# Optimization experiments

Hardware: AMD Instinct MI355X
Metric: run time of the kernel (lower is better)

Reference implementation:

```python
import jax, jax.numpy as jnp
import numpy as np

D = 1024          # embeddings_dims
HS = 128          # head_size = D // no_of_q_heads(=8)
NKV = 2           # hardcoded self.no_of_kv_heads = 2 (number of query Linear layers)


def apply_rope(x):
    # x: [..., T, d]; pairs of adjacent elements rotated (faithful to RotaryEmbeddings)
    d = x.shape[-1]
    T = x.shape[-2]
    positions = jnp.arange(0, d, 2, dtype=jnp.float32)           # step-2 positions (as in source)
    theta = 10000.0 ** (-2.0 * positions / d)                    # [d/2]
    angles = jnp.arange(T, dtype=jnp.float32)[:, None] * theta[None, :]  # [T, d/2]
    cos, sin = jnp.cos(angles), jnp.sin(angles)
    xr = x.reshape(x.shape[:-1] + (d // 2, 2))
    out = jnp.stack([xr[..., 0] * cos - xr[..., 1] * sin,
                     xr[..., 1] * cos + xr[..., 0] * sin], axis=-1)
    return out.reshape(x.shape)


def setup_inputs() -> dict:
    key = jax.random.key(0)
    k1, k2, k3, k4, k5 = jax.random.split(key, 5)
    B, T = 4, 2048
    x = jax.random.normal(k1, (B, T, D), dtype=jnp.float32)
    s = 1.0 / np.sqrt(D)
    Wq = jax.random.normal(k2, (NKV, HS, D), dtype=jnp.float32) * s  # 2 query Linear layers [out,in]
    Wk = jax.random.normal(k3, (HS, D), dtype=jnp.float32) * s
    Wv = jax.random.normal(k4, (HS, D), dtype=jnp.float32) * s
    Wo = jax.random.normal(k5, (D, NKV * HS), dtype=jnp.float32) * (1.0 / np.sqrt(NKV * HS))
    return {"x": x, "Wq": Wq, "Wk": Wk, "Wv": Wv, "Wo": Wo}


def reference(x, Wq, Wk, Wv, Wo):
    B, T, _ = x.shape
    k = apply_rope(x @ Wk.T)                              # [B,T,HS]
    v = x @ Wv.T                                          # [B,T,HS]
    q = jnp.einsum('btd,hkd->bhtk', x, Wq)                # [B,2,T,HS]
    q = apply_rope(q)
    scale = HS ** (-0.5)
    scores = jnp.einsum('bhtk,bsk->bhts', q, k) * scale   # [B,2,T,T]
    causal = jnp.tril(jnp.ones((T, T), dtype=bool))
    scores = jnp.where(causal, scores, -jnp.inf)
    w = jax.nn.softmax(scores, axis=-1)                   # dropout is identity at eval
    out = jnp.einsum('bhts,bsk->bhtk', w, v)              # [B,2,T,HS]
    out = out.transpose(0, 2, 1, 3).reshape(B, T, NKV * HS)  # concat heads on last dim
    return out @ Wo.T                                     # [B,T,D]
```

## Files before the change

### kernel.cpp

```cpp
#include <hip/hip_runtime.h>
#include <math.h>

#define DD 1024
#define HSZ 128
#define NB 4
#define TT 2048

typedef __attribute__((ext_vector_type(8))) short bf16x8;
typedef __attribute__((ext_vector_type(4))) float f32x4;

typedef __attribute__((address_space(3))) unsigned int lds_u32_t;
typedef __attribute__((address_space(1))) unsigned int glb_u32_t;

__device__ inline void gll16(const void* g, void* l) {
    __builtin_amdgcn_global_load_lds((const glb_u32_t*)g, (lds_u32_t*)l, 16, 0, 0);
}

__device__ inline unsigned short f2bf(float f){
    unsigned u = __builtin_bit_cast(unsigned, f);
    u += 0x7fff + ((u >> 16) & 1);
    return (unsigned short)(u >> 16);
}

__global__ __launch_bounds__(256) void prep_kernel(
    const float* __restrict__ Wq, const float* __restrict__ Wk,
    const float* __restrict__ Wv, const float* __restrict__ Wo,
    unsigned short* __restrict__ Wbp, unsigned short* __restrict__ Wop,
    float2* __restrict__ tab)
{
    int bid = blockIdx.x, tid = threadIdx.x;
    if (bid < 512) {
        int i = bid * 256 + tid;
        int t = i >> 6, j = i & 63;
        float theta = __powf(10000.f, -(float)j * (1.f / 32.f));
        float ang = (float)t * theta;
        tab[i] = make_float2(__cosf(ang), __sinf(ang));
        return;
    }
    const float* s;
    unsigned short* dst;
    if (bid < 768) {
        int gc = (bid - 512) * 256 + tid;
        int tileid = gc >> 10;
        int ct = tileid >> 4, kk = tileid & 15;
        int ch = gc & 1023;
        int ns = ch >> 7, kc = (ch >> 6) & 1, l6 = ch & 63;
        int wrow = ct * 128 + ns * 16 + (l6 & 15);
        int kcol = kk * 64 + kc * 32 + (l6 >> 4) * 8;
        s = (wrow < 256) ? Wq + (size_t)wrow * DD
          : (wrow < 384) ? Wk + (size_t)(wrow - 256) * DD
                         : Wv + (size_t)(wrow - 384) * DD;
        s += kcol;
        dst = Wbp + (size_t)gc * 8;
    } else {
        int gc = (bid - 768) * 256 + tid;
        int tileid = gc >> 10;
        int ct = tileid >> 2, kk = tileid & 3;
        int ch = gc & 1023;
        int ns = ch >> 7, kc = (ch >> 6) & 1, l6 = ch & 63;
        int orow = ct * 128 + ns * 16 + (l6 & 15);
        int kcol = kk * 64 + kc * 32 + (l6 >> 4) * 8;
        s = Wo + (size_t)orow * 256 + kcol;
        dst = Wop + (size_t)gc * 8;
    }
    float4 a = ((const float4*)s)[0];
    float4 c = ((const float4*)s)[1];
    unsigned short o[8] = {f2bf(a.x),f2bf(a.y),f2bf(a.z),f2bf(a.w),
                           f2bf(c.x),f2bf(c.y),f2bf(c.z),f2bf(c.w)};
    *(uint4*)dst = *(const uint4*)o;
}

__global__ __launch_bounds__(256) void qkv_gemm_kernel(
    const float* __restrict__ x,
    const unsigned short* __restrict__ Wbp,
    const float2* __restrict__ tab,
    unsigned short* __restrict__ qo,
    unsigned short* __restrict__ Kp,
    unsigned short* __restrict__ Vp)
{
    int bid = blockIdx.x;
    int rt = bid & 127, ct = bid >> 7;
    int row0 = rt * 64;
    int b = row0 >> 11, t0 = row0 & (TT - 1);
    int tid = threadIdx.x;
    int wave = tid >> 6, lane = tid & 63;
    int mrow = lane & 15, quad = lane >> 4;

    __shared__ unsigned short Bs[2][8192];

    f32x4 acc[8];
    #pragma unroll
    for (int ns = 0; ns < 8; ++ns)
        #pragma unroll
        for (int r = 0; r < 4; ++r) acc[ns][r] = 0.f;

    const float* xrow = x + (size_t)(row0 + wave * 16 + mrow) * DD;

    {
        const unsigned short* wt = Wbp + (size_t)(ct * 16) * 8192;
        #pragma unroll
        for (int u = 0; u < 4; ++u)
            gll16(wt + (size_t)(u * 256 + tid) * 8, &Bs[0][(u * 256 + (tid & 192)) * 8]);
    }

    for (int kk = 0; kk < 16; ++kk) {
        __syncthreads();
        if (kk < 15) {
            const unsigned short* wt = Wbp + (size_t)(ct * 16 + kk + 1) * 8192;
            #pragma unroll
            for (int u = 0; u < 4; ++u)
                gll16(wt + (size_t)(u * 256 + tid) * 8, &Bs[(kk + 1) & 1][(u * 256 + (tid & 192)) * 8]);
        }
        bf16x8 af[2];
        #pragma unroll
        for (int kc = 0; kc < 2; ++kc) {
            const float* s = xrow + kk * 64 + kc * 32 + quad * 8;
            float4 f0 = ((const float4*)s)[0];
            float4 f1 = ((const float4*)s)[1];
            bf16x8 pk;
            pk[0]=(short)f2bf(f0.x); pk[1]=(short)f2bf(f0.y); pk[2]=(short)f2bf(f0.z); pk[3]=(short)f2bf(f0.w);
            pk[4]=(short)f2bf(f1.x); pk[5]=(short)f2bf(f1.y); pk[6]=(short)f2bf(f1.z); pk[7]=(short)f2bf(f1.w);
            af[kc] = pk;
        }
        const unsigned short* Bcur = Bs[kk & 1];
        #pragma unroll
        for (int kc = 0; kc < 2; ++kc)
            #pragma unroll
            for (int ns = 0; ns < 8; ++ns) {
                bf16x8 bb = *(const bf16x8*)(Bcur + ((ns * 2 + kc) * 64 + lane) * 8);
                acc[ns] = __builtin_amdgcn_mfma_f32_16x16x32_bf16(af[kc], bb, acc[ns], 0, 0, 0);
            }
    }

    __syncthreads();

    if (ct < 2) {
        unsigned short* dst = qo + (size_t)(b * 2 + ct) * TT * HSZ;
        #pragma unroll
        for (int ns = 0; ns < 8; ++ns) {
            int colloc = ns * 16 + mrow;
            int pj = colloc >> 1;
            #pragma unroll
            for (int r = 0; r < 4; ++r) {
                int t = t0 + wave * 16 + quad * 4 + r;
                float v = acc[ns][r];
                float vp = __shfl_xor(v, 1, 64);
                float2 cs = tab[t * 64 + pj];
                float outv = ((mrow & 1) == 0) ? (v * cs.x - vp * cs.y)
                                               : (v * cs.x + vp * cs.y);
                dst[(size_t)t * HSZ + colloc] = f2bf(outv);
            }
        }
    } else if (ct == 2) {
        unsigned short* A_ = (unsigned short*)Bs;
        #pragma unroll
        for (int ns = 0; ns < 8; ++ns) {
            int colloc = ns * 16 + mrow;
            int pj = colloc >> 1;
            int chunk = (ns >> 1) * 4 + wave;
            int lph = (ns & 1) * 2 + (mrow >> 3);
            #pragma unroll
            for (int r = 0; r < 4; ++r) {
                int t = t0 + wave * 16 + quad * 4 + r;
                float v = acc[ns][r];
                float vp = __shfl_xor(v, 1, 64);
                float2 cs = tab[t * 64 + pj];
                float outv = ((mrow & 1) == 0) ? (v * cs.x - vp * cs.y)
                                               : (v * cs.x + vp * cs.y);
                A_[chunk * 512 + (lph * 16 + quad * 4 + r) * 8 + (mrow & 7)] = f2bf(outv);
            }
        }
        __syncthreads();
        unsigned short* kd = Kp + (size_t)(b * 32 + (t0 >> 6)) * 8192;
        #pragma unroll
        for (int u = 0; u < 4; ++u)
            *(uint4*)(kd + (u * 256 + tid) * 8) = *(const uint4*)(A_ + (u * 256 + tid) * 8);
    } else {
        unsigned short* A_ = (unsigned short*)Bs;
        #pragma unroll
        for (int ns = 0; ns < 8; ++ns) {
            int chunk = ns * 2 + (wave >> 1);
            int lanep = ((wave & 1) * 2 + (quad >> 1)) * 16 + mrow;
            #pragma unroll
            for (int r = 0; r < 4; ++r)
                A_[chunk * 512 + lanep * 8 + (quad & 1) * 4 + r] = f2bf(acc[ns][r]);
        }
        __syncthreads();
        unsigned short* vd = Vp + (size_t)(b * 32 + (t0 >> 6)) * 8192;
        #pragma unroll
        for (int u = 0; u < 4; ++u)
            *(uint4*)(vd + (u * 256 + tid) * 8) = *(const uint4*)(A_ + (u * 256 + tid) * 8);
    }
}

__global__ __launch_bounds__(256) void attn_mfma_kernel(
    const unsigned short* __restrict__ q,
    const unsigned short* __restrict__ Kp,
    const unsigned short* __restrict__ Vp,
    unsigned short* __restrict__ att)
{
    int bid = blockIdx.x;
    int rr = bid >> 3;
    int qt = (rr < 32) ? rr : 63 - (rr - 32);
    int bh = bid & 7;
    int b = bh >> 1, h = bh & 1;
    int q0 = qt * 32;
    int tid = threadIdx.x;
    int wave = tid >> 6, lane = tid & 63;
    int qsub = wave >> 1, par = wave & 1;
    int qw0 = q0 + qsub * 16;
    int mrow = lane & 15, quad = lane >> 4;

    __shared__ char raw[74240];
    unsigned short* Ks0 = (unsigned short*)raw;
    unsigned short* Vs0 = (unsigned short*)(raw + 32768);
    unsigned short* Psb = (unsigned short*)(raw + 65536);
    float* Ms_ = (float*)(raw + 73728);
    float* Ls_ = Ms_ + 32;
    float* Os  = (float*)raw;

    const unsigned short* qrow = q + (((size_t)(b * 2 + h)) * TT + qw0 + mrow) * HSZ + quad * 8;
    bf16x8 qf[4];
    #pragma unroll
    for (int c = 0; c < 4; ++c) qf[c] = *(const bf16x8*)(qrow + 32 * c);

    float mrun[4], lrun[4];
    f32x4 O[8];
    #pragma unroll
    for (int r = 0; r < 4; ++r) { mrun[r] = -1e30f; lrun[r] = 0.f; }
    #pragma unroll
    for (int g = 0; g < 8; ++g)
        #pragma unroll
        for (int r = 0; r < 4; ++r) O[g][r] = 0.f;

    const int NT = (qt + 2) >> 1;
    const float scl = 0.08838834764831845f;

    for (int jj = 0; jj < NT; jj += 2) {
        __syncthreads();
        for (int tp = 0; tp < 2; ++tp) {
            int j = jj + tp;
            if (j >= NT) break;
            const unsigned short* ks = Kp + (size_t)(b * 32 + j) * 8192;
            const unsigned short* vs = Vp + (size_t)(b * 32 + j) * 8192;
            #pragma unroll
            for (int u = 0; u < 4; ++u) {
                gll16(ks + (size_t)(u * 256 + tid) * 8, Ks0 + (tp * 8192) + (u * 256 + (tid & 192)) * 8);
                gll16(vs + (size_t)(u * 256 + tid) * 8, Vs0 + (tp * 8192) + (u * 256 + (tid & 192)) * 8);
            }
        }
        __syncthreads();

        int j = jj + par;
        int s0 = j * 64;
        if (j < NT && s0 <= qw0 + 15) {
            const unsigned short* Kt = Ks0 + par * 8192;
            const unsigned short* Vtt = Vs0 + par * 8192;

            f32x4 S[4];
            #pragma unroll
            for (int f = 0; f < 4; ++f)
                #pragma unroll
                for (int r = 0; r < 4; ++r) S[f][r] = 0.f;

            #pragma unroll
            for (int c = 0; c < 4; ++c)
                #pragma unroll
                for (int f = 0; f < 4; ++f) {
                    bf16x8 bk = *(const bf16x8*)(Kt + ((c * 4 + f) * 64 + lane) * 8);
                    S[f] = __builtin_amdgcn_mfma_f32_16x16x32_bf16(qf[c], bk, S[f], 0, 0, 0);
                }

            #pragma unroll
            for (int f = 0; f < 4; ++f) {
                int sg = s0 + 16 * f + mrow;
                #pragma unroll
                for (int r = 0; r < 4; ++r) {
                    int qg = qw0 + quad * 4 + r;
                    float val = S[f][r] * scl;
                    S[f][r] = (sg <= qg) ? val : -1e30f;
                }
            }

            float al[4];
            #pragma unroll
            for (int r = 0; r < 4; ++r) {
                float v = fmaxf(fmaxf(S[0][r], S[1][r]), fmaxf(S[2][r], S[3][r]));
                v = fmaxf(v, __shfl_xor(v, 1, 64));
                v = fmaxf(v, __shfl_xor(v, 2, 64));
                v = fmaxf(v, __shfl_xor(v, 4, 64));
                v = fmaxf(v, __shfl_xor(v, 8, 64));
                float mn = fmaxf(mrun[r], v);
                al[r] = __expf(mrun[r] - mn);
                mrun[r] = mn;
            }
            #pragma unroll
            for (int f = 0; f < 4; ++f)
                #pragma unroll
                for (int r = 0; r < 4; ++r)
                    S[f][r] = __expf(S[f][r] - mrun[r]);
            #pragma unroll
            for (int r = 0; r < 4; ++r) {
                float v = (S[0][r] + S[1][r]) + (S[2][r] + S[3][r]);
                v += __shfl_xor(v, 1, 64);
                v += __shfl_xor(v, 2, 64);
                v += __shfl_xor(v, 4, 64);
                v += __shfl_xor(v, 8, 64);
                lrun[r] = lrun[r] * al[r] + v;
            }
            #pragma unroll
            for (int g = 0; g < 8; ++g) {
                O[g][0] *= al[0]; O[g][1] *= al[1]; O[g][2] *= al[2]; O[g][3] *= al[3];
            }

            unsigned short* Pw = Psb + wave * 1024;
            #pragma unroll
            for (int f = 0; f < 4; ++f) {
                int p = f >> 1;
                int hi2 = (2 * f + (mrow >> 3)) & 3;
                int jlo = mrow & 7;
                #pragma unroll
                for (int r = 0; r < 4; ++r)
                    Pw[(p * 64 + hi2 * 16 + quad * 4 + r) * 8 + jlo] = f2bf(S[f][r]);
            }
            bf16x8 pa[2];
            pa[0] = *(const bf16x8*)(Pw + lane * 8);
            pa[1] = *(const bf16x8*)(Pw + (64 + lane) * 8);

            #pragma unroll
            for (int g = 0; g < 8; ++g)
                #pragma unroll
                for (int p = 0; p < 2; ++p) {
                    bf16x8 bv = *(const bf16x8*)(Vtt + ((g * 2 + p) * 64 + lane) * 8);
                    O[g] = __builtin_amdgcn_mfma_f32_16x16x32_bf16(pa[p], bv, O[g], 0, 0, 0);
                }
        }
    }

    __syncthreads();
    if (par == 1) {
        if (mrow == 0) {
            #pragma unroll
            for (int r = 0; r < 4; ++r) {
                Ms_[qsub * 16 + quad * 4 + r] = mrun[r];
                Ls_[qsub * 16 + quad * 4 + r] = lrun[r];
            }
        }
        float* Ow = Os + qsub * 2048;
        #pragma unroll
        for (int g = 0; g < 8; ++g)
            #pragma unroll
            for (int r = 0; r < 4; ++r)
                Ow[(quad * 4 + r) * 128 + g * 16 + mrow] = O[g][r];
    }
    __syncthreads();
    if (par == 0) {
        const float* Op = Os + qsub * 2048;
        float A0[4], A1[4], inv[4];
        #pragma unroll
        for (int r = 0; r < 4; ++r) {
            float m1 = Ms_[qsub * 16 + quad * 4 + r];
            float l1 = Ls_[qsub * 16 + quad * 4 + r];
            float m12 = fmaxf(mrun[r], m1);
            A0[r] = __expf(mrun[r] - m12);
            A1[r] = __expf(m1 - m12);
            inv[r] = 1.f / (lrun[r] * A0[r] + l1 * A1[r]);
        }
        unsigned short* ab = att + (((size_t)b * TT + qw0) * 2 + h) * 128;
        #pragma unroll
        for (int g = 0; g < 8; ++g)
            #pragma unroll
            for (int r = 0; r < 4; ++r) {
                int row = quad * 4 + r;
                float o = (O[g][r] * A0[r] + Op[row * 128 + g * 16 + mrow] * A1[r]) * inv[r];
                ab[(size_t)row * 256 + g * 16 + mrow] = f2bf(o);
            }
    }
}

__global__ __launch_bounds__(256) void outproj_gemm_kernel(
    const unsigned short* __restrict__ attb,
    const unsigned short* __restrict__ Wop,
    float* __restrict__ y)
{
    int bid = blockIdx.x;
    int rt = bid & 127, ct = bid >> 7;
    int row0 = rt * 64;
    int tid = threadIdx.x;
    int wave = tid >> 6, lane = tid & 63;
    int mrow = lane & 15, quad = lane >> 4;

    __shared__ unsigned short Bs[2][8192];

    f32x4 acc[8];
    #pragma unroll
    for (int ns = 0; ns < 8; ++ns)
        #pragma unroll
        for (int r = 0; r < 4; ++r) acc[ns][r] = 0.f;

    const unsigned short* arow = attb + (size_t)(row0 + wave * 16 + mrow) * 256;

    {
        const unsigned short* wt = Wop + (size_t)(ct * 4) * 8192;
        #pragma unroll
        for (int u = 0; u < 4; ++u)
            gll16(wt + (size_t)(u * 256 + tid) * 8, &Bs[0][(u * 256 + (tid & 192)) * 8]);
    }

    for (int kk = 0; kk < 4; ++kk) {
        __syncthreads();
        if (kk < 3) {
            const unsigned short* wt = Wop + (size_t)(ct * 4 + kk + 1) * 8192;
            #pragma unroll
            for (int u = 0; u < 4; ++u)
                gll16(wt + (size_t)(u * 256 + tid) * 8, &Bs[(kk + 1) & 1][(u * 256 + (tid & 192)) * 8]);
        }
        const unsigned short* Bcur = Bs[kk & 1];
        #pragma unroll
        for (int kc = 0; kc < 2; ++kc) {
            bf16x8 af = *(const bf16x8*)(arow + kk * 64 + kc * 32 + quad * 8);
            #pragma unroll
            for (int ns = 0; ns < 8; ++ns) {
                bf16x8 bb = *(const bf16x8*)(Bcur + ((ns * 2 + kc) * 64 + lane) * 8);
                acc[ns] = __builtin_amdgcn_mfma_f32_16x16x32_bf16(af, bb, acc[ns], 0, 0, 0);
            }
        }
    }

    #pragma unroll
    for (int ns = 0; ns < 8; ++ns)
        #pragma unroll
        for (int r = 0; r < 4; ++r) {
            int row = row0 + wave * 16 + quad * 4 + r;
            y[(size_t)row * DD + ct * 128 + ns * 16 + mrow] = acc[ns][r];
        }
}

extern "C" void kernel_launch(void* const* d_in, const int* in_sizes, int n_in,
                              void* d_out, int out_size, void* d_ws, size_t ws_size,
                              hipStream_t stream) {
    const float* x  = (const float*)d_in[0];
    const float* Wq = (const float*)d_in[1];
    const float* Wk = (const float*)d_in[2];
    const float* Wv = (const float*)d_in[3];
    const float* Wo = (const float*)d_in[4];
    float* y = (float*)d_out;

    char* ws = (char*)d_ws;
    unsigned short* at  = (unsigned short*)(ws);
    unsigned short* qo  = (unsigned short*)(ws + 4u  * 1024 * 1024);
    unsigned short* Kp  = (unsigned short*)(ws + 8u  * 1024 * 1024);
    unsigned short* Vp  = (unsigned short*)(ws + 10u * 1024 * 1024);
    unsigned short* Wbp = (unsigned short*)(ws + 12u * 1024 * 1024);
    unsigned short* Wop = (unsigned short*)(ws + 13u * 1024 * 1024);
    float2*         tb  = (float2*)        (ws + 13824u * 1024);

    prep_kernel<<<896, 256, 0, stream>>>(Wq, Wk, Wv, Wo, Wbp, Wop, tb);
    qkv_gemm_kernel<<<512, 256, 0, stream>>>(x, Wbp, tb, qo, Kp, Vp);
    attn_mfma_kernel<<<512, 256, 0, stream>>>(qo, Kp, Vp, at);
    outproj_gemm_kernel<<<1024, 256, 0, stream>>>(at, Wop, y);
}
```

Baseline: 169.6 us.

## Split attention KV tiles across four waves, each covering 32 query rows

The attention kernel now assigns key/value tiles round-robin to the four waves, and each wave handles all 32 query rows of the block. Each wave reads K and V tiles straight from global memory instead of staging them through LDS, which removes the per-iteration block-wide barriers. Partial softmax results from the four waves are merged through LDS at the end. The block order now runs from the longest query tile to the shortest, the causal mask is applied only on the last tile, and the launch bounds request two blocks per CU. The cost is more registers per wave, redundant global reads of K/V with no LDS reuse, and a four-way final merge.

```diff
diff --git a/kernel.cpp b/kernel.cpp
--- a/kernel.cpp
+++ b/kernel.cpp
@@ -193,127 +193,127 @@
     }
 }
 
-__global__ __launch_bounds__(256) void attn_mfma_kernel(
+__global__ __launch_bounds__(256, 2) void attn_mfma_kernel(
     const unsigned short* __restrict__ q,
     const unsigned short* __restrict__ Kp,
     const unsigned short* __restrict__ Vp,
     unsigned short* __restrict__ att)
 {
     int bid = blockIdx.x;
-    int rr = bid >> 3;
-    int qt = (rr < 32) ? rr : 63 - (rr - 32);
+    int qt = 63 - (bid >> 3);
     int bh = bid & 7;
     int b = bh >> 1, h = bh & 1;
     int q0 = qt * 32;
     int tid = threadIdx.x;
     int wave = tid >> 6, lane = tid & 63;
-    int qsub = wave >> 1, par = wave & 1;
-    int qw0 = q0 + qsub * 16;
     int mrow = lane & 15, quad = lane >> 4;
 
-    __shared__ char raw[74240];
-    unsigned short* Ks0 = (unsigned short*)raw;
-    unsigned short* Vs0 = (unsigned short*)(raw + 32768);
-    unsigned short* Psb = (unsigned short*)(raw + 65536);
-    float* Ms_ = (float*)(raw + 73728);
-    float* Ls_ = Ms_ + 32;
-    float* Os  = (float*)raw;
-
-    const unsigned short* qrow = q + (((size_t)(b * 2 + h)) * TT + qw0 + mrow) * HSZ + quad * 8;
-    bf16x8 qf[4];
+    __shared__ char raw[66304];
+    unsigned short* Psb = (unsigned short*)raw;
+    float* Os  = (float*)(raw + 16384);
+    float* Ms_ = (float*)(raw + 65536);
+    float* Ls_ = Ms_ + 96;
+
+    const unsigned short* qbase = q + (((size_t)(b * 2 + h)) * TT + q0 + mrow) * HSZ + quad * 8;
+    bf16x8 qf[2][4];
     #pragma unroll
-    for (int c = 0; c < 4; ++c) qf[c] = *(const bf16x8*)(qrow + 32 * c);
-
-    float mrun[4], lrun[4];
-    f32x4 O[8];
+    for (int u = 0; u < 2; ++u)
+        #pragma unroll
+        for (int c = 0; c < 4; ++c)
+            qf[u][c] = *(const bf16x8*)(qbase + u * 16 * HSZ + 32 * c);
+
+    float mrun[2][4], lrun[2][4];
+    f32x4 O[2][8];
     #pragma unroll
-    for (int r = 0; r < 4; ++r) { mrun[r] = -1e30f; lrun[r] = 0.f; }
-    #pragma unroll
-    for (int g = 0; g < 8; ++g)
-        #pragma unroll
-        for (int r = 0; r < 4; ++r) O[g][r] = 0.f;
-
-    const int NT = (qt + 2) >> 1;
+    for (int u = 0; u < 2; ++u) {
+        #pragma unroll
+        for (int r = 0; r < 4; ++r) { mrun[u][r] = -1e30f; lrun[u][r] = 0.f; }
+        #pragma unroll
+        for (int g = 0; g < 8; ++g)
+            #pragma unroll
+            for (int r = 0; r < 4; ++r) O[u][g][r] = 0.f;
+    }
+
+    const int NT = (qt >> 1) + 1;
     const float scl = 0.08838834764831845f;
-
-    for (int jj = 0; jj < NT; jj += 2) {
-        __syncthreads();
-        for (int tp = 0; tp < 2; ++tp) {
-            int j = jj + tp;
-            if (j >= NT) break;
-            const unsigned short* ks = Kp + (size_t)(b * 32 + j) * 8192;
-            const unsigned short* vs = Vp + (size_t)(b * 32 + j) * 8192;
-            #pragma unroll
-            for (int u = 0; u < 4; ++u) {
-                gll16(ks + (size_t)(u * 256 + tid) * 8, Ks0 + (tp * 8192) + (u * 256 + (tid & 192)) * 8);
-                gll16(vs + (size_t)(u * 256 + tid) * 8, Vs0 + (tp * 8192) + (u * 256 + (tid & 192)) * 8);
-            }
-        }
-        __syncthreads();
-
-        int j = jj + par;
+    unsigned short* Pw = Psb + wave * 2048;
+
+    for (int j = wave; j < NT; j += 4) {
+        const unsigned short* Kt = Kp + (size_t)(b * 32 + j) * 8192;
+        const unsigned short* Vt = Vp + (size_t)(b * 32 + j) * 8192;
         int s0 = j * 64;
-        if (j < NT && s0 <= qw0 + 15) {
-            const unsigned short* Kt = Ks0 + par * 8192;
-            const unsigned short* Vtt = Vs0 + par * 8192;
-
-            f32x4 S[4];
+
+        f32x4 S[2][4];
+        #pragma unroll
+        for (int u = 0; u < 2; ++u)
             #pragma unroll
             for (int f = 0; f < 4; ++f)
                 #pragma unroll
-                for (int r = 0; r < 4; ++r) S[f][r] = 0.f;
-
-            #pragma unroll
-            for (int c = 0; c < 4; ++c)
+                for (int r = 0; r < 4; ++r) S[u][f][r] = 0.f;
+
+        #pragma unroll
+        for (int c = 0; c < 4; ++c)
+            #pragma unroll
+            for (int f = 0; f < 4; ++f) {
+                bf16x8 bk = *(const bf16x8*)(Kt + ((c * 4 + f) * 64 + lane) * 8);
+                S[0][f] = __builtin_amdgcn_mfma_f32_16x16x32_bf16(qf[0][c], bk, S[0][f], 0, 0, 0);
+                S[1][f] = __builtin_amdgcn_mfma_f32_16x16x32_bf16(qf[1][c], bk, S[1][f], 0, 0, 0);
+            }
+
+        if (j == NT - 1) {
+            #pragma unroll
+            for (int u = 0; u < 2; ++u)
                 #pragma unroll
                 for (int f = 0; f < 4; ++f) {
-                    bf16x8 bk = *(const bf16x8*)(Kt + ((c * 4 + f) * 64 + lane) * 8);
-                    S[f] = __builtin_amdgcn_mfma_f32_16x16x32_bf16(qf[c], bk, S[f], 0, 0, 0);
+                    int sg = s0 + 16 * f + mrow;
+                    #pragma unroll
+                    for (int r = 0; r < 4; ++r) {
+                        int qg = q0 + u * 16 + quad * 4 + r;
+                        S[u][f][r] = (sg <= qg) ? S[u][f][r] * scl : -1e30f;
+                    }
                 }
-
-            #pragma unroll
-            for (int f = 0; f < 4; ++f) {
-                int sg = s0 + 16 * f + mrow;
-                #pragma unroll
-                for (int r = 0; r < 4; ++r) {
-                    int qg = qw0 + quad * 4 + r;
-                    float val = S[f][r] * scl;
-                    S[f][r] = (sg <= qg) ? val : -1e30f;
-                }
-            }
-
+        } else {
+            #pragma unroll
+            for (int u = 0; u < 2; ++u)
+                #pragma unroll
+                for (int f = 0; f < 4; ++f)
+                    #pragma unroll
+                    for (int r = 0; r < 4; ++r) S[u][f][r] *= scl;
+        }
+
+        #pragma unroll
+        for (int u = 0; u < 2; ++u) {
             float al[4];
             #pragma unroll
             for (int r = 0; r < 4; ++r) {
-                float v = fmaxf(fmaxf(S[0][r], S[1][r]), fmaxf(S[2][r], S[3][r]));
+                float v = fmaxf(fmaxf(S[u][0][r], S[u][1][r]), fmaxf(S[u][2][r], S[u][3][r]));
                 v = fmaxf(v, __shfl_xor(v, 1, 64));
                 v = fmaxf(v, __shfl_xor(v, 2, 64));
                 v = fmaxf(v, __shfl_xor(v, 4, 64));
                 v = fmaxf(v, __shfl_xor(v, 8, 64));
-                float mn = fmaxf(mrun[r], v);
-                al[r] = __expf(mrun[r] - mn);
-                mrun[r] = mn;
+                float mn = fmaxf(mrun[u][r], v);
+                al[r] = __expf(mrun[u][r] - mn);
+                mrun[u][r] = mn;
             }
             #pragma unroll
             for (int f = 0; f < 4; ++f)
                 #pragma unroll
                 for (int r = 0; r < 4; ++r)
-                    S[f][r] = __expf(S[f][r] - mrun[r]);
+                    S[u][f][r] = __expf(S[u][f][r] - mrun[u][r]);
             #pragma unroll
             for (int r = 0; r < 4; ++r) {
-                float v = (S[0][r] + S[1][r]) + (S[2][r] + S[3][r]);
+                float v = (S[u][0][r] + S[u][1][r]) + (S[u][2][r] + S[u][3][r]);
                 v += __shfl_xor(v, 1, 64);
                 v += __shfl_xor(v, 2, 64);
                 v += __shfl_xor(v, 4, 64);
                 v += __shfl_xor(v, 8, 64);
-                lrun[r] = lrun[r] * al[r] + v;
+                lrun[u][r] = lrun[u][r] * al[r] + v;
             }
             #pragma unroll
             for (int g = 0; g < 8; ++g) {
-                O[g][0] *= al[0]; O[g][1] *= al[1]; O[g][2] *= al[2]; O[g][3] *= al[3];
-            }
-
-            unsigned short* Pw = Psb + wave * 1024;
+                O[u][g][0] *= al[0]; O[u][g][1] *= al[1];
+                O[u][g][2] *= al[2]; O[u][g][3] *= al[3];
+            }
             #pragma unroll
             for (int f = 0; f < 4; ++f) {
                 int p = f >> 1;
@@ -321,60 +321,76 @@
                 int jlo = mrow & 7;
                 #pragma unroll
                 for (int r = 0; r < 4; ++r)
-                    Pw[(p * 64 + hi2 * 16 + quad * 4 + r) * 8 + jlo] = f2bf(S[f][r]);
-            }
-            bf16x8 pa[2];
-            pa[0] = *(const bf16x8*)(Pw + lane * 8);
-            pa[1] = *(const bf16x8*)(Pw + (64 + lane) * 8);
-
+                    Pw[u * 1024 + (p * 64 + hi2 * 16 + quad * 4 + r) * 8 + jlo] = f2bf(S[u][f][r]);
+            }
+        }
+
+        bf16x8 pa[2][2];
+        #pragma unroll
+        for (int u = 0; u < 2; ++u)
+            #pragma unroll
+            for (int p = 0; p < 2; ++p)
+                pa[u][p] = *(const bf16x8*)(Pw + u * 1024 + (p * 64 + lane) * 8);
+
+        #pragma unroll
+        for (int g = 0; g < 8; ++g)
+            #pragma unroll
+            for (int p = 0; p < 2; ++p) {
+                bf16x8 bv = *(const bf16x8*)(Vt + ((g * 2 + p) * 64 + lane) * 8);
+                O[0][g] = __builtin_amdgcn_mfma_f32_16x16x32_bf16(pa[0][p], bv, O[0][g], 0, 0, 0);
+                O[1][g] = __builtin_amdgcn_mfma_f32_16x16x32_bf16(pa[1][p], bv, O[1][g], 0, 0, 0);
+            }
+    }
+
+    if (wave) {
+        float* Ow = Os + (wave - 1) * 4096;
+        #pragma unroll
+        for (int u = 0; u < 2; ++u)
             #pragma unroll
             for (int g = 0; g < 8; ++g)
                 #pragma unroll
-                for (int p = 0; p < 2; ++p) {
-                    bf16x8 bv = *(const bf16x8*)(Vtt + ((g * 2 + p) * 64 + lane) * 8);
-                    O[g] = __builtin_amdgcn_mfma_f32_16x16x32_bf16(pa[p], bv, O[g], 0, 0, 0);
+                for (int r = 0; r < 4; ++r)
+                    Ow[(u * 16 + quad * 4 + r) * 128 + g * 16 + mrow] = O[u][g][r];
+        if (mrow == 0) {
+            #pragma unroll
+            for (int u = 0; u < 2; ++u)
+                #pragma unroll
+                for (int r = 0; r < 4; ++r) {
+                    Ms_[(wave - 1) * 32 + u * 16 + quad * 4 + r] = mrun[u][r];
+                    Ls_[(wave - 1) * 32 + u * 16 + quad * 4 + r] = lrun[u][r];
                 }
         }
     }
-
     __syncthreads();
-    if (par == 1) {
-        if (mrow == 0) {
+    if (wave == 0) {
+        unsigned short* ab = att + (((size_t)b * TT + q0) * 2 + h) * 128;
+        #pragma unroll
+        for (int u = 0; u < 2; ++u) {
+            float a0[4], a1[4], a2[4], a3[4], inv[4];
             #pragma unroll
             for (int r = 0; r < 4; ++r) {
-                Ms_[qsub * 16 + quad * 4 + r] = mrun[r];
-                Ls_[qsub * 16 + quad * 4 + r] = lrun[r];
-            }
-        }
-        float* Ow = Os + qsub * 2048;
-        #pragma unroll
-        for (int g = 0; g < 8; ++g)
-            #pragma unroll
-            for (int r = 0; r < 4; ++r)
-                Ow[(quad * 4 + r) * 128 + g * 16 + mrow] = O[g][r];
-    }
-    __syncthreads();
-    if (par == 0) {
-        const float* Op = Os + qsub * 2048;
-        float A0[4], A1[4], inv[4];
-        #pragma unroll
-        for (int r = 0; r < 4; ++r) {
-            float m1 = Ms_[qsub * 16 + quad * 4 + r];
-            float l1 = Ls_[qsub * 16 + quad * 4 + r];
-            float m12 = fmaxf(mrun[r], m1);
-            A0[r] = __expf(mrun[r] - m12);
-            A1[r] = __expf(m1 - m12);
-            inv[r] = 1.f / (lrun[r] * A0[r] + l1 * A1[r]);
-        }
-        unsigned short* ab = att + (((size_t)b * TT + qw0) * 2 + h) * 128;
-        #pragma unroll
-        for (int g = 0; g < 8; ++g)
-            #pragma unroll
-            for (int r = 0; r < 4; ++r) {
-                int row = quad * 4 + r;
-                float o = (O[g][r] * A0[r] + Op[row * 128 + g * 16 + mrow] * A1[r]) * inv[r];
-                ab[(size_t)row * 256 + g * 16 + mrow] = f2bf(o);
-            }
+                int row = u * 16 + quad * 4 + r;
+                float m0 = mrun[u][r], l0 = lrun[u][r];
+                float m1 = Ms_[row],      l1 = Ls_[row];
+                float m2 = Ms_[32 + row], l2 = Ls_[32 + row];
+                float m3 = Ms_[64 + row], l3 = Ls_[64 + row];
+                float mM = fmaxf(fmaxf(m0, m1), fmaxf(m2, m3));
+                a0[r] = __expf(m0 - mM); a1[r] = __expf(m1 - mM);
+                a2[r] = __expf(m2 - mM); a3[r] = __expf(m3 - mM);
+                inv[r] = 1.f / (l0 * a0[r] + l1 * a1[r] + l2 * a2[r] + l3 * a3[r]);
+            }
+            #pragma unroll
+            for (int g = 0; g < 8; ++g)
+                #pragma unroll
+                for (int r = 0; r < 4; ++r) {
+                    int row = u * 16 + quad * 4 + r;
+                    float o = O[u][g][r] * a0[r]
+                            + Os[row * 128 + g * 16 + mrow] * a1[r]
+                            + Os[4096 + row * 128 + g * 16 + mrow] * a2[r]
+                            + Os[8192 + row * 128 + g * 16 + mrow] * a3[r];
+                    ab[(size_t)row * 256 + g * 16 + mrow] = f2bf(o * inv[r]);
+                }
+        }
     }
 }
 
```

New measurement: 159.4 us. 6.1% less time.

## Split attention KV tiles across four waves per 16-row query block

Applied to the files above, without the earlier changes.

Each attention block now covers 16 query rows instead of 32, and its four waves each process every fourth KV tile, reading K/V directly from global memory instead of staging them through LDS. Partial softmax states are merged through a two-level LDS tree reduction. The softmax scale is folded into Q in the projection epilogue, the causal mask is applied only on the diagonal tile, and the P scratch buffer uses an XOR swizzle. The grid doubles to 1024 blocks and LDS use drops so more blocks can fit per CU, at the cost of K/V reuse across waves and extra merge work.

```diff
diff --git a/kernel.cpp b/kernel.cpp
--- a/kernel.cpp
+++ b/kernel.cpp
@@ -21,6 +21,8 @@
     u += 0x7fff + ((u >> 16) & 1);
     return (unsigned short)(u >> 16);
 }
+
+#define QSCL 0.08838834764831845f
 
 __global__ __launch_bounds__(256) void prep_kernel(
     const float* __restrict__ Wq, const float* __restrict__ Wk,
@@ -148,7 +150,7 @@
                 float2 cs = tab[t * 64 + pj];
                 float outv = ((mrow & 1) == 0) ? (v * cs.x - vp * cs.y)
                                                : (v * cs.x + vp * cs.y);
-                dst[(size_t)t * HSZ + colloc] = f2bf(outv);
+                dst[(size_t)t * HSZ + colloc] = f2bf(outv * QSCL);
             }
         }
     } else if (ct == 2) {
@@ -193,36 +195,34 @@
     }
 }
 
-__global__ __launch_bounds__(256) void attn_mfma_kernel(
+__global__ __launch_bounds__(256, 4) void attn_mfma_kernel(
     const unsigned short* __restrict__ q,
     const unsigned short* __restrict__ Kp,
     const unsigned short* __restrict__ Vp,
     unsigned short* __restrict__ att)
 {
     int bid = blockIdx.x;
-    int rr = bid >> 3;
-    int qt = (rr < 32) ? rr : 63 - (rr - 32);
+    int t = bid >> 3;
+    int s_ = t >> 5, r_ = t & 31;
+    int qt = (s_ == 0) ? r_ : (s_ == 1) ? 63 - r_ : (s_ == 2) ? 64 + r_ : 127 - r_;
     int bh = bid & 7;
     int b = bh >> 1, h = bh & 1;
-    int q0 = qt * 32;
+    int q0 = qt * 16;
     int tid = threadIdx.x;
     int wave = tid >> 6, lane = tid & 63;
-    int qsub = wave >> 1, par = wave & 1;
-    int qw0 = q0 + qsub * 16;
     int mrow = lane & 15, quad = lane >> 4;
 
-    __shared__ char raw[74240];
-    unsigned short* Ks0 = (unsigned short*)raw;
-    unsigned short* Vs0 = (unsigned short*)(raw + 32768);
-    unsigned short* Psb = (unsigned short*)(raw + 65536);
-    float* Ms_ = (float*)(raw + 73728);
-    float* Ls_ = Ms_ + 32;
-    float* Os  = (float*)raw;
-
-    const unsigned short* qrow = q + (((size_t)(b * 2 + h)) * TT + qw0 + mrow) * HSZ + quad * 8;
+    __shared__ char raw[16640];
+    unsigned short* Psb = (unsigned short*)raw;
+    float* bufA = (float*)raw;
+    float* bufB = (float*)(raw + 8192);
+    float* Ms_  = (float*)(raw + 16384);
+    float* Ls_  = Ms_ + 32;
+
+    const unsigned short* qbase = q + (((size_t)(b * 2 + h)) * TT + q0 + mrow) * HSZ + quad * 8;
     bf16x8 qf[4];
     #pragma unroll
-    for (int c = 0; c < 4; ++c) qf[c] = *(const bf16x8*)(qrow + 32 * c);
+    for (int c = 0; c < 4; ++c) qf[c] = *(const bf16x8*)(qbase + 32 * c);
 
     float mrun[4], lrun[4];
     f32x4 O[8];
@@ -233,146 +233,171 @@
         #pragma unroll
         for (int r = 0; r < 4; ++r) O[g][r] = 0.f;
 
-    const int NT = (qt + 2) >> 1;
-    const float scl = 0.08838834764831845f;
-
-    for (int jj = 0; jj < NT; jj += 2) {
-        __syncthreads();
-        for (int tp = 0; tp < 2; ++tp) {
-            int j = jj + tp;
-            if (j >= NT) break;
-            const unsigned short* ks = Kp + (size_t)(b * 32 + j) * 8192;
-            const unsigned short* vs = Vp + (size_t)(b * 32 + j) * 8192;
-            #pragma unroll
-            for (int u = 0; u < 4; ++u) {
-                gll16(ks + (size_t)(u * 256 + tid) * 8, Ks0 + (tp * 8192) + (u * 256 + (tid & 192)) * 8);
-                gll16(vs + (size_t)(u * 256 + tid) * 8, Vs0 + (tp * 8192) + (u * 256 + (tid & 192)) * 8);
-            }
-        }
-        __syncthreads();
-
-        int j = jj + par;
+    const int NT = (qt >> 2) + 1;
+    unsigned short* Pw = Psb + wave * 1024;
+
+    for (int j = wave; j < NT; j += 4) {
+        const unsigned short* Kt = Kp + (size_t)(b * 32 + j) * 8192;
+        const unsigned short* Vt = Vp + (size_t)(b * 32 + j) * 8192;
         int s0 = j * 64;
-        if (j < NT && s0 <= qw0 + 15) {
-            const unsigned short* Kt = Ks0 + par * 8192;
-            const unsigned short* Vtt = Vs0 + par * 8192;
-
-            f32x4 S[4];
-            #pragma unroll
-            for (int f = 0; f < 4; ++f)
-                #pragma unroll
-                for (int r = 0; r < 4; ++r) S[f][r] = 0.f;
-
-            #pragma unroll
-            for (int c = 0; c < 4; ++c)
-                #pragma unroll
-                for (int f = 0; f < 4; ++f) {
-                    bf16x8 bk = *(const bf16x8*)(Kt + ((c * 4 + f) * 64 + lane) * 8);
-                    S[f] = __builtin_amdgcn_mfma_f32_16x16x32_bf16(qf[c], bk, S[f], 0, 0, 0);
-                }
-
+
+        f32x4 S[4];
+        #pragma unroll
+        for (int f = 0; f < 4; ++f)
+            #pragma unroll
+            for (int r = 0; r < 4; ++r) S[f][r] = 0.f;
+
+        #pragma unroll
+        for (int c = 0; c < 4; ++c)
+            #pragma unroll
+            for (int f = 0; f < 4; ++f) {
+                bf16x8 bk = *(const bf16x8*)(Kt + ((c * 4 + f) * 64 + lane) * 8);
+                S[f] = __builtin_amdgcn_mfma_f32_16x16x32_bf16(qf[c], bk, S[f], 0, 0, 0);
+            }
+
+        if (j == NT - 1) {
             #pragma unroll
             for (int f = 0; f < 4; ++f) {
                 int sg = s0 + 16 * f + mrow;
                 #pragma unroll
                 for (int r = 0; r < 4; ++r) {
-                    int qg = qw0 + quad * 4 + r;
-                    float val = S[f][r] * scl;
-                    S[f][r] = (sg <= qg) ? val : -1e30f;
+                    int qg = q0 + quad * 4 + r;
+                    S[f][r] = (sg <= qg) ? S[f][r] : -1e30f;
                 }
             }
-
-            float al[4];
+        }
+
+        float al[4];
+        #pragma unroll
+        for (int r = 0; r < 4; ++r) {
+            float v = fmaxf(fmaxf(S[0][r], S[1][r]), fmaxf(S[2][r], S[3][r]));
+            v = fmaxf(v, __shfl_xor(v, 1, 64));
+            v = fmaxf(v, __shfl_xor(v, 2, 64));
+            v = fmaxf(v, __shfl_xor(v, 4, 64));
+            v = fmaxf(v, __shfl_xor(v, 8, 64));
+            float mn = fmaxf(mrun[r], v);
+            al[r] = __expf(mrun[r] - mn);
+            mrun[r] = mn;
+        }
+        #pragma unroll
+        for (int f = 0; f < 4; ++f)
+            #pragma unroll
+            for (int r = 0; r < 4; ++r)
+                S[f][r] = __expf(S[f][r] - mrun[r]);
+        #pragma unroll
+        for (int r = 0; r < 4; ++r) {
+            float v = (S[0][r] + S[1][r]) + (S[2][r] + S[3][r]);
+            v += __shfl_xor(v, 1, 64);
+            v += __shfl_xor(v, 2, 64);
+            v += __shfl_xor(v, 4, 64);
+            v += __shfl_xor(v, 8, 64);
+            lrun[r] = lrun[r] * al[r] + v;
+        }
+        #pragma unroll
+        for (int g = 0; g < 8; ++g) {
+            O[g][0] *= al[0]; O[g][1] *= al[1]; O[g][2] *= al[2]; O[g][3] *= al[3];
+        }
+        #pragma unroll
+        for (int f = 0; f < 4; ++f) {
+            int p = f >> 1;
+            int hi2 = (2 * f + (mrow >> 3)) & 3;
+            int jlo = mrow & 7;
+            int gx = (quad >> 1) | (hi2 << 1);
             #pragma unroll
             for (int r = 0; r < 4; ++r) {
-                float v = fmaxf(fmaxf(S[0][r], S[1][r]), fmaxf(S[2][r], S[3][r]));
-                v = fmaxf(v, __shfl_xor(v, 1, 64));
-                v = fmaxf(v, __shfl_xor(v, 2, 64));
-                v = fmaxf(v, __shfl_xor(v, 4, 64));
-                v = fmaxf(v, __shfl_xor(v, 8, 64));
-                float mn = fmaxf(mrun[r], v);
-                al[r] = __expf(mrun[r] - mn);
-                mrun[r] = mn;
-            }
-            #pragma unroll
-            for (int f = 0; f < 4; ++f)
+                int idx = p * 64 + hi2 * 16 + quad * 4 + r;
+                Pw[(idx ^ gx) * 8 + jlo] = f2bf(S[f][r]);
+            }
+        }
+
+        bf16x8 pa[2];
+        #pragma unroll
+        for (int p = 0; p < 2; ++p) {
+            int li = p * 64 + lane;
+            int si = li ^ ((li >> 3) & 7);
+            pa[p] = *(const bf16x8*)(Pw + si * 8);
+        }
+
+        #pragma unroll
+        for (int g = 0; g < 8; ++g)
+            #pragma unroll
+            for (int p = 0; p < 2; ++p) {
+                bf16x8 bv = *(const bf16x8*)(Vt + ((g * 2 + p) * 64 + lane) * 8);
+                O[g] = __builtin_amdgcn_mfma_f32_16x16x32_bf16(pa[p], bv, O[g], 0, 0, 0);
+            }
+    }
+
+    __syncthreads();
+    if (wave & 1) {
+        float* buf = (wave == 1) ? bufA : bufB;
+        int base = (wave == 1) ? 0 : 16;
+        #pragma unroll
+        for (int g = 0; g < 8; ++g)
+            #pragma unroll
+            for (int r = 0; r < 4; ++r)
+                buf[(quad * 4 + r) * 128 + g * 16 + mrow] = O[g][r];
+        if (mrow == 0) {
+            #pragma unroll
+            for (int r = 0; r < 4; ++r) {
+                Ms_[base + quad * 4 + r] = mrun[r];
+                Ls_[base + quad * 4 + r] = lrun[r];
+            }
+        }
+    }
+    __syncthreads();
+    if ((wave & 1) == 0) {
+        float* buf = (wave == 0) ? bufA : bufB;
+        int base = (wave == 0) ? 0 : 16;
+        float a0[4], a1[4];
+        #pragma unroll
+        for (int r = 0; r < 4; ++r) {
+            int row = quad * 4 + r;
+            float m1 = Ms_[base + row], l1 = Ls_[base + row];
+            float mM = fmaxf(mrun[r], m1);
+            a0[r] = __expf(mrun[r] - mM);
+            a1[r] = __expf(m1 - mM);
+            mrun[r] = mM;
+            lrun[r] = lrun[r] * a0[r] + l1 * a1[r];
+        }
+        #pragma unroll
+        for (int g = 0; g < 8; ++g)
+            #pragma unroll
+            for (int r = 0; r < 4; ++r)
+                O[g][r] = O[g][r] * a0[r] + buf[(quad * 4 + r) * 128 + g * 16 + mrow] * a1[r];
+        if (wave == 2) {
+            #pragma unroll
+            for (int g = 0; g < 8; ++g)
                 #pragma unroll
                 for (int r = 0; r < 4; ++r)
-                    S[f][r] = __expf(S[f][r] - mrun[r]);
-            #pragma unroll
-            for (int r = 0; r < 4; ++r) {
-                float v = (S[0][r] + S[1][r]) + (S[2][r] + S[3][r]);
-                v += __shfl_xor(v, 1, 64);
-                v += __shfl_xor(v, 2, 64);
-                v += __shfl_xor(v, 4, 64);
-                v += __shfl_xor(v, 8, 64);
-                lrun[r] = lrun[r] * al[r] + v;
-            }
-            #pragma unroll
-            for (int g = 0; g < 8; ++g) {
-                O[g][0] *= al[0]; O[g][1] *= al[1]; O[g][2] *= al[2]; O[g][3] *= al[3];
-            }
-
-            unsigned short* Pw = Psb + wave * 1024;
-            #pragma unroll
-            for (int f = 0; f < 4; ++f) {
-                int p = f >> 1;
-                int hi2 = (2 * f + (mrow >> 3)) & 3;
-                int jlo = mrow & 7;
+                    bufB[(quad * 4 + r) * 128 + g * 16 + mrow] = O[g][r];
+            if (mrow == 0) {
                 #pragma unroll
-                for (int r = 0; r < 4; ++r)
-                    Pw[(p * 64 + hi2 * 16 + quad * 4 + r) * 8 + jlo] = f2bf(S[f][r]);
-            }
-            bf16x8 pa[2];
-            pa[0] = *(const bf16x8*)(Pw + lane * 8);
-            pa[1] = *(const bf16x8*)(Pw + (64 + lane) * 8);
-
-            #pragma unroll
-            for (int g = 0; g < 8; ++g)
-                #pragma unroll
-                for (int p = 0; p < 2; ++p) {
-                    bf16x8 bv = *(const bf16x8*)(Vtt + ((g * 2 + p) * 64 + lane) * 8);
-                    O[g] = __builtin_amdgcn_mfma_f32_16x16x32_bf16(pa[p], bv, O[g], 0, 0, 0);
+                for (int r = 0; r < 4; ++r) {
+                    Ms_[16 + quad * 4 + r] = mrun[r];
+                    Ls_[16 + quad * 4 + r] = lrun[r];
                 }
-        }
-    }
-
+            }
+        }
+    }
     __syncthreads();
-    if (par == 1) {
-        if (mrow == 0) {
-            #pragma unroll
-            for (int r = 0; r < 4; ++r) {
-                Ms_[qsub * 16 + quad * 4 + r] = mrun[r];
-                Ls_[qsub * 16 + quad * 4 + r] = lrun[r];
-            }
-        }
-        float* Ow = Os + qsub * 2048;
-        #pragma unroll
-        for (int g = 0; g < 8; ++g)
-            #pragma unroll
-            for (int r = 0; r < 4; ++r)
-                Ow[(quad * 4 + r) * 128 + g * 16 + mrow] = O[g][r];
-    }
-    __syncthreads();
-    if (par == 0) {
-        const float* Op = Os + qsub * 2048;
-        float A0[4], A1[4], inv[4];
+    if (wave == 0) {
+        unsigned short* ab = att + (((size_t)b * TT + q0) * 2 + h) * 128;
+        float a0[4], a2[4], inv[4];
         #pragma unroll
         for (int r = 0; r < 4; ++r) {
-            float m1 = Ms_[qsub * 16 + quad * 4 + r];
-            float l1 = Ls_[qsub * 16 + quad * 4 + r];
-            float m12 = fmaxf(mrun[r], m1);
-            A0[r] = __expf(mrun[r] - m12);
-            A1[r] = __expf(m1 - m12);
-            inv[r] = 1.f / (lrun[r] * A0[r] + l1 * A1[r]);
-        }
-        unsigned short* ab = att + (((size_t)b * TT + qw0) * 2 + h) * 128;
+            int row = quad * 4 + r;
+            float m2 = Ms_[16 + row], l2 = Ls_[16 + row];
+            float mM = fmaxf(mrun[r], m2);
+            a0[r] = __expf(mrun[r] - mM);
+            a2[r] = __expf(m2 - mM);
+            inv[r] = 1.f / (lrun[r] * a0[r] + l2 * a2[r]);
+        }
         #pragma unroll
         for (int g = 0; g < 8; ++g)
             #pragma unroll
             for (int r = 0; r < 4; ++r) {
                 int row = quad * 4 + r;
-                float o = (O[g][r] * A0[r] + Op[row * 128 + g * 16 + mrow] * A1[r]) * inv[r];
+                float o = (O[g][r] * a0[r] + bufB[row * 128 + g * 16 + mrow] * a2[r]) * inv[r];
                 ab[(size_t)row * 256 + g * 16 + mrow] = f2bf(o);
             }
     }
@@ -457,6 +482,6 @@
 
     prep_kernel<<<896, 256, 0, stream>>>(Wq, Wk, Wv, Wo, Wbp, Wop, tb);
     qkv_gemm_kernel<<<512, 256, 0, stream>>>(x, Wbp, tb, qo, Kp, Vp);
-    attn_mfma_kernel<<<512, 256, 0, stream>>>(qo, Kp, Vp, at);
+    attn_mfma_kernel<<<1024, 256, 0, stream>>>(qo, Kp, Vp, at);
     outproj_gemm_kernel<<<1024, 256, 0, stream>>>(at, Wop, y);
 }
```

Result: slower. 196.7 us (+15.9%).
